# Performance work log

Measured on AMD Instinct MI355X. Metric: run time of the kernel, lower is better.

## Reference

```python
import jax, jax.numpy as jnp
import numpy as np

B, H, S, DK = 2, 16, 2048, 64

def setup_inputs() -> dict:
    key = jax.random.key(0)
    kq, kk, kv = jax.random.split(key, 3)
    shape = (B, H, S, DK)
    return {
        "multi_head_q": jax.random.normal(kq, shape, dtype=jnp.float32),
        "multi_head_k": jax.random.normal(kk, shape, dtype=jnp.float32),
        "multi_head_v": jax.random.normal(kv, shape, dtype=jnp.float32),
    }

def reference(multi_head_q, multi_head_k, multi_head_v):
    d_k = multi_head_q.shape[-1]
    scale = 1.0 / jnp.sqrt(jnp.asarray(d_k, dtype=multi_head_q.dtype))
    # scores: [B, H, S, S]
    scores = jnp.einsum("bhqd,bhkd->bhqk", multi_head_q, multi_head_k) * scale
    attn = jax.nn.softmax(scores, axis=-1)
    # z: [B, H, S, DK]
    z = jnp.einsum("bhqk,bhkd->bhqd", attn, multi_head_v)
    # transpose heads to [B, S, H, DK] then merge -> [B, S, H*DK]
    b, h, s, d = z.shape
    return jnp.swapaxes(z, 1, 2).reshape(b, s, h * d)
```

## Files before the change

### kernel.cpp

```cpp
#include <hip/hip_runtime.h>
#include <cmath>


#define S_LEN   2048
#define D_HEAD  64
#define NHEADS  16
#define NBH     32
#define TQ      128
#define TK      32
#define NTILE   (S_LEN / TK)
#define NSTREAM 2
#define HTILE   (NTILE / NSTREAM)
#define LDSTR   72
#define TILE_SH (TK * D_HEAD)
#define PAIR_SH 4096

typedef short bfrag8 __attribute__((ext_vector_type(8)));
typedef float f32x4  __attribute__((ext_vector_type(4)));
typedef float f32x16 __attribute__((ext_vector_type(16)));
typedef int   i32x2  __attribute__((ext_vector_type(2)));
typedef int   i32x4  __attribute__((ext_vector_type(4)));

static __device__ __forceinline__ int pk2bf(float a, float b) {
  unsigned short lo = __builtin_bit_cast(unsigned short, (__bf16)a);
  unsigned short hi = __builtin_bit_cast(unsigned short, (__bf16)b);
  return (int)lo | ((int)hi << 16);
}

static __device__ __forceinline__ float fexp2(float x) {
#if __has_builtin(__builtin_amdgcn_exp2f)
  return __builtin_amdgcn_exp2f(x);
#else
  return exp2f(x);
#endif
}

static __device__ __forceinline__ void gload_lds16(const short* g, short* l) {
  __builtin_amdgcn_global_load_lds(
      (const __attribute__((address_space(1))) void*)g,
      (__attribute__((address_space(3))) void*)l, 16, 0, 0);
}

__global__ __launch_bounds__(256)
void fa_prep(const float* __restrict__ K, const float* __restrict__ V,
             short* __restrict__ Kt, short* __restrict__ Vt) {
  __shared__ float fl[64][65];

  const int tid = threadIdx.x;
  int id = blockIdx.x;
  const bool isV = id >= NBH * (NTILE / 2);
  if (isV) id -= NBH * (NTILE / 2);
  const int xcd = id & 7;
  const int s   = id >> 3;
  const int bh  = xcd * 4 + (s >> 5);
  const int t   = s & 31;

  const size_t ibase = ((size_t)bh * S_LEN + t * 64) * D_HEAD;

  if (!isV) {
    short* kt = Kt + (size_t)(bh * (NTILE / 2) + t) * PAIR_SH;
#pragma unroll
    for (int p = 0; p < 2; ++p) {
      int idx = p * 256 + tid;
      int key = idx >> 3, c = idx & 7;
      const float* src = K + ibase + key * 64 + c * 8;
      float4 a = *(const float4*)src;
      float4 b = *(const float4*)(src + 4);
      i32x4 w;
      w[0] = pk2bf(a.x, a.y); w[1] = pk2bf(a.z, a.w);
      w[2] = pk2bf(b.x, b.y); w[3] = pk2bf(b.z, b.w);
      *(i32x4*)(kt + key * 64 + ((c ^ (key & 7)) * 8)) = w;
    }
  } else {
    short* vt = Vt + (size_t)(bh * (NTILE / 2) + t) * PAIR_SH;
#pragma unroll
    for (int i = 0; i < 4; ++i) {
      int e = (i * 256 + tid) * 4;
      int row = e >> 6, col = e & 63;
      float4 v = *(const float4*)(V + ibase + (size_t)row * 64 + col);
      fl[col + 0][row] = v.x;
      fl[col + 1][row] = v.y;
      fl[col + 2][row] = v.z;
      fl[col + 3][row] = v.w;
    }
    __syncthreads();
#pragma unroll
    for (int p = 0; p < 2; ++p) {
      int idx = p * 256 + tid;
      int d = idx >> 3, ck = idx & 7;
      const float* row = &fl[d][ck * 8];
      i32x4 w;
      w[0] = pk2bf(row[0], row[1]); w[1] = pk2bf(row[2], row[3]);
      w[2] = pk2bf(row[4], row[5]); w[3] = pk2bf(row[6], row[7]);
      short* dst = vt + (ck >> 2) * TILE_SH + d * 32
                      + (((ck & 3) ^ ((d >> 1) & 3)) * 8);
      *(i32x4*)dst = w;
    }
  }
}

__global__ __launch_bounds__(512, 4)
void fa_fwd3(const float* __restrict__ Q, const short* __restrict__ Kt,
             const short* __restrict__ Vt, float* __restrict__ Out) {
  __shared__ short SM[2 * NSTREAM * 3 * TILE_SH];
  short* KsS = SM;
  short* VsS = SM + NSTREAM * 3 * TILE_SH;

  const int tid    = threadIdx.x;
  const int wid    = tid >> 6;
  const int stream = wid >> 2;
  const int qw     = wid & 3;
  const int lane   = tid & 63;
  const int h      = lane >> 5;
  const int c      = lane & 31;
  const int c7     = c & 7;
  const int c13    = (c >> 1) & 3;
  const int qb     = 32 * qw;
  const int s3     = stream * 3;

  const int id   = blockIdx.x;
  const int xcd  = id & 7;
  const int slot = id >> 3;
  const int bh   = xcd * 4 + (slot >> 4);
  const int q0   = (slot & 15) * 128;

  const int t0   = stream * HTILE;

  const float qscale = 0.125f * 1.44269504088896340736f;

  const float* Qg = Q + ((size_t)bh * S_LEN + (q0 + qb + c)) * D_HEAD;
  bfrag8 qf[4];
#pragma unroll
  for (int sl = 0; sl < 4; ++sl) {
    const float* qp = Qg + 16 * sl + 8 * h;
    float4 a = *(const float4*)qp;
    float4 b = *(const float4*)(qp + 4);
    i32x4 w;
    w[0] = pk2bf(a.x * qscale, a.y * qscale);
    w[1] = pk2bf(a.z * qscale, a.w * qscale);
    w[2] = pk2bf(b.x * qscale, b.y * qscale);
    w[3] = pk2bf(b.z * qscale, b.w * qscale);
    qf[sl] = __builtin_bit_cast(bfrag8, w);
  }

  const short* ktb = Kt + (size_t)bh * NTILE * TILE_SH;
  const short* vtb = Vt + (size_t)bh * NTILE * TILE_SH;

  auto stage = [&](int b, int gt) {
    const short* ksrc = ktb + (size_t)gt * TILE_SH;
    const short* vsrc = vtb + (size_t)gt * TILE_SH;
    const int ch = qw * 512;
    gload_lds16(ksrc + ch + lane * 8, &KsS[(s3 + b) * TILE_SH + ch]);
    gload_lds16(vsrc + ch + lane * 8, &VsS[(s3 + b) * TILE_SH + ch]);
  };

  f32x16 acc[2];
#pragma unroll
  for (int m = 0; m < 2; ++m)
#pragma unroll
    for (int i = 0; i < 16; ++i) acc[m][i] = 0.f;

  float lrun = 0.f;

  auto compute = [&](const short* ksb, const short* vsb) {
    f32x16 st;
#pragma unroll
    for (int i = 0; i < 16; ++i) st[i] = 0.f;

    __builtin_amdgcn_s_setprio(1);
#pragma unroll
    for (int sl = 0; sl < 4; ++sl) {
      bfrag8 af = *(const bfrag8*)&ksb[c * 64 + (((2 * sl + h) ^ c7) * 8)];
      st = __builtin_amdgcn_mfma_f32_32x32x16_bf16(af, qf[sl], st, 0, 0, 0);
    }
    __builtin_amdgcn_s_setprio(0);

    float ls = 0.f;
#pragma unroll
    for (int i = 0; i < 16; ++i) {
      st[i] = fexp2(st[i]);
      ls += st[i];
    }
    lrun += ls;

    bfrag8 pf[2];
#pragma unroll
    for (int hf = 0; hf < 2; ++hf) {
      const int b0 = 8 * hf;
      int w0 = pk2bf(st[b0 + 0], st[b0 + 1]);
      int w1 = pk2bf(st[b0 + 2], st[b0 + 3]);
      int w2 = pk2bf(st[b0 + 4], st[b0 + 5]);
      int w3 = pk2bf(st[b0 + 6], st[b0 + 7]);
      asm("v_permlane32_swap_b32 %0, %1" : "+v"(w0), "+v"(w2));
      asm("v_permlane32_swap_b32 %0, %1" : "+v"(w1), "+v"(w3));
      i32x4 f; f[0] = w0; f[1] = w1; f[2] = w2; f[3] = w3;
      pf[hf] = __builtin_bit_cast(bfrag8, f);
    }

    __builtin_amdgcn_s_setprio(1);
#pragma unroll
    for (int sl2 = 0; sl2 < 2; ++sl2) {
#pragma unroll
      for (int mtd = 0; mtd < 2; ++mtd) {
        bfrag8 av = *(const bfrag8*)
            &vsb[(32 * mtd + c) * 32 + (((2 * sl2 + h) ^ c13) * 8)];
        acc[mtd] = __builtin_amdgcn_mfma_f32_32x32x16_bf16(av, pf[sl2], acc[mtd], 0, 0, 0);
      }
    }
    __builtin_amdgcn_s_setprio(0);
  };

  stage(0, t0 + 0);
  stage(1, t0 + 1);
  int cur = 0;
  for (int t = 0; t < HTILE; ++t) {
    if (t + 1 < HTILE) asm volatile("s_waitcnt vmcnt(2)" ::: "memory");
    else               asm volatile("s_waitcnt vmcnt(0)" ::: "memory");
    __builtin_amdgcn_s_barrier();
    __builtin_amdgcn_sched_barrier(0);
    if (t + 2 < HTILE) {
      int b2 = cur + 2; if (b2 >= 3) b2 -= 3;
      stage(b2, t0 + t + 2);
    }
    compute(&KsS[(s3 + cur) * TILE_SH], &VsS[(s3 + cur) * TILE_SH]);
    if (++cur == 3) cur = 0;
  }

  float* red = (float*)SM;
  const int rbase = (qw * 64 + lane) * 33;
  __syncthreads();
  if (stream == 1) {
#pragma unroll
    for (int i = 0; i < 16; ++i) red[rbase + i]      = acc[0][i];
#pragma unroll
    for (int i = 0; i < 16; ++i) red[rbase + 16 + i] = acc[1][i];
    red[rbase + 32] = lrun;
  }
  __syncthreads();
  if (stream == 0) {
#pragma unroll
    for (int i = 0; i < 16; ++i) acc[0][i] += red[rbase + i];
#pragma unroll
    for (int i = 0; i < 16; ++i) acc[1][i] += red[rbase + 16 + i];
    lrun += red[rbase + 32];
    float l = lrun + __shfl_xor(lrun, 32);
    float inv = 1.0f / l;
    const int bb = bh >> 4, hh = bh & 15;
    const int qg = q0 + qb + c;
    float* op = Out + ((size_t)bb * S_LEN + qg) * (NHEADS * D_HEAD) + hh * D_HEAD;
#pragma unroll
    for (int mtd = 0; mtd < 2; ++mtd)
#pragma unroll
      for (int g = 0; g < 4; ++g) {
        float4 o;
        o.x = acc[mtd][4 * g + 0] * inv;
        o.y = acc[mtd][4 * g + 1] * inv;
        o.z = acc[mtd][4 * g + 2] * inv;
        o.w = acc[mtd][4 * g + 3] * inv;
        *(float4*)(op + 32 * mtd + 8 * g + 4 * h) = o;
      }
  }
}

__global__ __launch_bounds__(256, 2)
void fa_fwd(const float* __restrict__ Q, const float* __restrict__ K,
            const float* __restrict__ V, float* __restrict__ Out) {
  __shared__ short Ksf[2][64 * LDSTR];
  __shared__ short VsT[2][D_HEAD * LDSTR];
  __shared__ short Psf[TQ * LDSTR];

  const int tid  = threadIdx.x;
  const int wid  = tid >> 6;
  const int lane = tid & 63;
  const int quad = lane >> 4;
  const int r    = lane & 15;
  const int qb   = 32 * wid;

  const int bh = blockIdx.y;
  const int q0 = blockIdx.x * TQ;

  const float* Qg = Q + (size_t)bh * S_LEN * D_HEAD;
  const float* Kg = K + (size_t)bh * S_LEN * D_HEAD;
  const float* Vg = V + (size_t)bh * S_LEN * D_HEAD;

  const float qscale = 0.125f * 1.44269504088896340736f;

  bfrag8 qf[2][2];
#pragma unroll
  for (int nt = 0; nt < 2; ++nt)
#pragma unroll
    for (int ks = 0; ks < 2; ++ks) {
      const float* qp = Qg + (size_t)(q0 + qb + 16 * nt + r) * D_HEAD + 32 * ks + 8 * quad;
      float4 a = *(const float4*)qp;
      float4 b = *(const float4*)(qp + 4);
      i32x4 w;
      w[0] = pk2bf(a.x * qscale, a.y * qscale);
      w[1] = pk2bf(a.z * qscale, a.w * qscale);
      w[2] = pk2bf(b.x * qscale, b.y * qscale);
      w[3] = pk2bf(b.z * qscale, b.w * qscale);
      qf[nt][ks] = __builtin_bit_cast(bfrag8, w);
    }

  float4 kpre[4];
  float  vpre[16];

  auto load_tile = [&](int k0) {
#pragma unroll
    for (int i = 0; i < 4; ++i) {
      int e = (i * 256 + tid) * 4;
      kpre[i] = *(const float4*)(Kg + (size_t)(k0 + (e >> 6)) * D_HEAD + (e & 63));
    }
    const float* vpp = Vg + (size_t)(k0 + wid * 16) * D_HEAD + lane;
#pragma unroll
    for (int j = 0; j < 16; ++j) vpre[j] = vpp[(size_t)j * D_HEAD];
  };

  auto store_tile = [&](short* ksb, short* vsb) {
#pragma unroll
    for (int i = 0; i < 4; ++i) {
      int e = (i * 256 + tid) * 4;
      i32x2 w;
      w[0] = pk2bf(kpre[i].x, kpre[i].y);
      w[1] = pk2bf(kpre[i].z, kpre[i].w);
      *(i32x2*)&ksb[(e >> 6) * LDSTR + (e & 63)] = w;
    }
    i32x4 w0, w1;
#pragma unroll
    for (int j = 0; j < 4; ++j) w0[j] = pk2bf(vpre[2 * j],     vpre[2 * j + 1]);
#pragma unroll
    for (int j = 0; j < 4; ++j) w1[j] = pk2bf(vpre[8 + 2 * j], vpre[9 + 2 * j]);
    *(i32x4*)&vsb[lane * LDSTR + wid * 16]     = w0;
    *(i32x4*)&vsb[lane * LDSTR + wid * 16 + 8] = w1;
  };

  f32x4 acc[4][2];
#pragma unroll
  for (int mt = 0; mt < 4; ++mt)
#pragma unroll
    for (int nt = 0; nt < 2; ++nt)
      acc[mt][nt] = (f32x4){0.f, 0.f, 0.f, 0.f};

  float lrun[2] = {0.f, 0.f};

  auto compute = [&](const short* ksb, const short* vsb) {
    f32x4 st[4][2];
#pragma unroll
    for (int mt = 0; mt < 4; ++mt)
#pragma unroll
      for (int nt = 0; nt < 2; ++nt)
        st[mt][nt] = (f32x4){0.f, 0.f, 0.f, 0.f};
#pragma unroll
    for (int ks = 0; ks < 2; ++ks) {
      bfrag8 af[4];
#pragma unroll
      for (int mt = 0; mt < 4; ++mt)
        af[mt] = *(const bfrag8*)&ksb[(r + 16 * mt) * LDSTR + quad * 8 + 32 * ks];
#pragma unroll
      for (int mt = 0; mt < 4; ++mt)
#pragma unroll
        for (int nt = 0; nt < 2; ++nt)
          st[mt][nt] = __builtin_amdgcn_mfma_f32_16x16x32_bf16(af[mt], qf[nt][ks], st[mt][nt], 0, 0, 0);
    }
#pragma unroll
    for (int nt = 0; nt < 2; ++nt) {
      float ssum = 0.f;
#pragma unroll
      for (int mt = 0; mt < 4; ++mt) {
        float p0 = fexp2(st[mt][nt][0]);
        float p1 = fexp2(st[mt][nt][1]);
        float p2 = fexp2(st[mt][nt][2]);
        float p3 = fexp2(st[mt][nt][3]);
        ssum += (p0 + p1) + (p2 + p3);
        i32x2 w;
        w[0] = pk2bf(p0, p1);
        w[1] = pk2bf(p2, p3);
        *(i32x2*)&Psf[(qb + 16 * nt + r) * LDSTR + 16 * mt + 4 * quad] = w;
      }
      lrun[nt] += ssum;
    }
#pragma unroll
    for (int ks = 0; ks < 2; ++ks) {
      bfrag8 av[4], bp[2];
#pragma unroll
      for (int mt = 0; mt < 4; ++mt)
        av[mt] = *(const bfrag8*)&vsb[(r + 16 * mt) * LDSTR + quad * 8 + 32 * ks];
#pragma unroll
      for (int nt = 0; nt < 2; ++nt)
        bp[nt] = *(const bfrag8*)&Psf[(qb + 16 * nt + r) * LDSTR + quad * 8 + 32 * ks];
#pragma unroll
      for (int mt = 0; mt < 4; ++mt)
#pragma unroll
        for (int nt = 0; nt < 2; ++nt)
          acc[mt][nt] = __builtin_amdgcn_mfma_f32_16x16x32_bf16(av[mt], bp[nt], acc[mt][nt], 0, 0, 0);
    }
  };

  load_tile(0);
  store_tile(Ksf[0], VsT[0]);
  load_tile(64);

  for (int it = 0; it < S_LEN / 64; it += 2) {
    __syncthreads();
    compute(Ksf[0], VsT[0]);
    store_tile(Ksf[1], VsT[1]);
    if (it + 2 < S_LEN / 64) load_tile((it + 2) * 64);
    __syncthreads();
    compute(Ksf[1], VsT[1]);
    if (it + 2 < S_LEN / 64) {
      store_tile(Ksf[0], VsT[0]);
      if (it + 3 < S_LEN / 64) load_tile((it + 3) * 64);
    }
  }

  const int bb = bh >> 4, hh = bh & 15;
#pragma unroll
  for (int nt = 0; nt < 2; ++nt) {
    float l = lrun[nt];
    l += __shfl_xor(l, 16);
    l += __shfl_xor(l, 32);
    float inv = 1.0f / l;
    int qg = q0 + qb + 16 * nt + r;
    float* op = Out + ((size_t)bb * S_LEN + qg) * (NHEADS * D_HEAD) + hh * D_HEAD;
#pragma unroll
    for (int mt = 0; mt < 4; ++mt) {
      float4 o;
      o.x = acc[mt][nt][0] * inv; o.y = acc[mt][nt][1] * inv;
      o.z = acc[mt][nt][2] * inv; o.w = acc[mt][nt][3] * inv;
      *(float4*)(op + 16 * mt + 4 * quad) = o;
    }
  }
}

extern "C" void kernel_launch(void* const* d_in, const int* in_sizes, int n_in,
                              void* d_out, int out_size, void* d_ws, size_t ws_size,
                              hipStream_t stream) {
  const float* Q = (const float*)d_in[0];
  const float* K = (const float*)d_in[1];
  const float* V = (const float*)d_in[2];
  float* O = (float*)d_out;

  const size_t telems = (size_t)NBH * NTILE * TILE_SH;
  const size_t need   = 2 * telems * sizeof(short);

  if (ws_size >= need) {
    short* Kt = (short*)d_ws;
    short* Vt = Kt + telems;
    fa_prep<<<dim3(NBH * NTILE), 256, 0, stream>>>(K, V, Kt, Vt);
    fa_fwd3<<<dim3(512), 512, 0, stream>>>(Q, Kt, Vt, O);
  } else {
    dim3 grid(S_LEN / TQ, NBH);
    fa_fwd<<<grid, 256, 0, stream>>>(Q, K, V, O);
  }
}
```

Baseline: 137.1 us.

## Software-pipeline QK of next tile with softmax and PV of previous tile

The main loop now issues the QK MFMAs for tile t before running exp, bf16 packing and the PV MFMAs for tile t-1, with scores alternating between two register sets. This lets matrix work overlap the exp and permlane work. The LDS ring grows from 3 to 4 buffers per stream so in-flight tiles are not overwritten, and LDS offsets are precomputed. The extra LDS (about 64 KB per block) and extra score registers may reduce how many blocks fit per CU.

```diff
diff --git a/kernel.cpp b/kernel.cpp
--- a/kernel.cpp
+++ b/kernel.cpp
@@ -102,9 +102,7 @@
 __global__ __launch_bounds__(512, 4)
 void fa_fwd3(const float* __restrict__ Q, const short* __restrict__ Kt,
              const short* __restrict__ Vt, float* __restrict__ Out) {
-  __shared__ short SM[2 * NSTREAM * 3 * TILE_SH];
-  short* KsS = SM;
-  short* VsS = SM + NSTREAM * 3 * TILE_SH;
+  __shared__ short SM[2 * NSTREAM * 4 * TILE_SH];
 
   const int tid    = threadIdx.x;
   const int wid    = tid >> 6;
@@ -116,7 +114,9 @@
   const int c7     = c & 7;
   const int c13    = (c >> 1) & 3;
   const int qb     = 32 * qw;
-  const int s3     = stream * 3;
+
+  short* ksReg = SM + stream * 4 * TILE_SH;
+  short* vsReg = SM + NSTREAM * 4 * TILE_SH + stream * 4 * TILE_SH;
 
   const int id   = blockIdx.x;
   const int xcd  = id & 7;
@@ -143,15 +143,25 @@
     qf[sl] = __builtin_bit_cast(bfrag8, w);
   }
 
+  int koff[4], voff[4];
+#pragma unroll
+  for (int sl = 0; sl < 4; ++sl)
+    koff[sl] = c * 64 + (((2 * sl + h) ^ c7) * 8);
+#pragma unroll
+  for (int sl2 = 0; sl2 < 2; ++sl2)
+#pragma unroll
+    for (int mtd = 0; mtd < 2; ++mtd)
+      voff[sl2 * 2 + mtd] = (32 * mtd + c) * 32 + (((2 * sl2 + h) ^ c13) * 8);
+
   const short* ktb = Kt + (size_t)bh * NTILE * TILE_SH;
   const short* vtb = Vt + (size_t)bh * NTILE * TILE_SH;
 
   auto stage = [&](int b, int gt) {
-    const short* ksrc = ktb + (size_t)gt * TILE_SH;
-    const short* vsrc = vtb + (size_t)gt * TILE_SH;
     const int ch = qw * 512;
-    gload_lds16(ksrc + ch + lane * 8, &KsS[(s3 + b) * TILE_SH + ch]);
-    gload_lds16(vsrc + ch + lane * 8, &VsS[(s3 + b) * TILE_SH + ch]);
+    gload_lds16(ktb + (size_t)gt * TILE_SH + ch + lane * 8,
+                ksReg + b * TILE_SH + ch);
+    gload_lds16(vtb + (size_t)gt * TILE_SH + ch + lane * 8,
+                vsReg + b * TILE_SH + ch);
   };
 
   f32x16 acc[2];
@@ -162,19 +172,20 @@
 
   float lrun = 0.f;
 
-  auto compute = [&](const short* ksb, const short* vsb) {
-    f32x16 st;
+  auto qk = [&](int b, f32x16& st) {
 #pragma unroll
     for (int i = 0; i < 16; ++i) st[i] = 0.f;
-
+    const short* kb = ksReg + b * TILE_SH;
     __builtin_amdgcn_s_setprio(1);
 #pragma unroll
     for (int sl = 0; sl < 4; ++sl) {
-      bfrag8 af = *(const bfrag8*)&ksb[c * 64 + (((2 * sl + h) ^ c7) * 8)];
+      bfrag8 af = *(const bfrag8*)&kb[koff[sl]];
       st = __builtin_amdgcn_mfma_f32_32x32x16_bf16(af, qf[sl], st, 0, 0, 0);
     }
     __builtin_amdgcn_s_setprio(0);
-
+  };
+
+  auto finish = [&](int b, f32x16& st) {
     float ls = 0.f;
 #pragma unroll
     for (int i = 0; i < 16; ++i) {
@@ -197,34 +208,37 @@
       pf[hf] = __builtin_bit_cast(bfrag8, f);
     }
 
+    const short* vb = vsReg + b * TILE_SH;
     __builtin_amdgcn_s_setprio(1);
 #pragma unroll
-    for (int sl2 = 0; sl2 < 2; ++sl2) {
+    for (int sl2 = 0; sl2 < 2; ++sl2)
 #pragma unroll
       for (int mtd = 0; mtd < 2; ++mtd) {
-        bfrag8 av = *(const bfrag8*)
-            &vsb[(32 * mtd + c) * 32 + (((2 * sl2 + h) ^ c13) * 8)];
+        bfrag8 av = *(const bfrag8*)&vb[voff[sl2 * 2 + mtd]];
         acc[mtd] = __builtin_amdgcn_mfma_f32_32x32x16_bf16(av, pf[sl2], acc[mtd], 0, 0, 0);
       }
-    }
     __builtin_amdgcn_s_setprio(0);
   };
 
   stage(0, t0 + 0);
   stage(1, t0 + 1);
-  int cur = 0;
+  f32x16 stA, stB;
+#pragma unroll 4
   for (int t = 0; t < HTILE; ++t) {
     if (t + 1 < HTILE) asm volatile("s_waitcnt vmcnt(2)" ::: "memory");
     else               asm volatile("s_waitcnt vmcnt(0)" ::: "memory");
     __builtin_amdgcn_s_barrier();
     __builtin_amdgcn_sched_barrier(0);
-    if (t + 2 < HTILE) {
-      int b2 = cur + 2; if (b2 >= 3) b2 -= 3;
-      stage(b2, t0 + t + 2);
-    }
-    compute(&KsS[(s3 + cur) * TILE_SH], &VsS[(s3 + cur) * TILE_SH]);
-    if (++cur == 3) cur = 0;
-  }
+    if (t + 2 < HTILE) stage((t + 2) & 3, t0 + t + 2);
+    if (t & 1) {
+      qk(t & 3, stB);
+      if (t > 0) finish((t - 1) & 3, stA);
+    } else {
+      qk(t & 3, stA);
+      if (t > 0) finish((t - 1) & 3, stB);
+    }
+  }
+  finish((HTILE - 1) & 3, stB);
 
   float* red = (float*)SM;
   const int rbase = (qw * 64 + lane) * 33;
```

After: 134.4 us. No clear change (-2.0%).
